# Kernel tuning notes

Hardware: AMD Instinct MI355X
Metric: run time of the kernel (lower is better)

The kernel has to match this reference:

```python
import jax, jax.numpy as jnp
import numpy as np

N = 50000
E = 800000
D_IN = 128
D_H = 128
N_CLASSES = 40
N_HIDDEN = 2


def _gcn_norm(edge_index, num_nodes):
    # Add self loops, compute symmetric normalization D^-1/2 (A+I) D^-1/2
    loops = jnp.arange(num_nodes, dtype=edge_index.dtype)
    src = jnp.concatenate([edge_index[0], loops])
    dst = jnp.concatenate([edge_index[1], loops])
    deg = jax.ops.segment_sum(jnp.ones_like(src, dtype=jnp.float32), dst,
                              num_segments=num_nodes)
    dinv = jnp.where(deg > 0, jax.lax.rsqrt(jnp.maximum(deg, 1.0)), 0.0)
    norm = dinv[src] * dinv[dst]  # [E+N]
    return src, dst, norm


def _gcn_conv(x, src, dst, norm, W, b):
    h = x @ W                          # [N, d_out] transform first (PyG order)
    msg = h[src] * norm[:, None]       # gather + scale, [E+N, d_out]
    out = jax.ops.segment_sum(msg, dst, num_segments=x.shape[0])
    return out + b


def setup_inputs() -> dict:
    key = jax.random.key(0)
    ks = jax.random.split(key, 8)
    x = jax.random.normal(ks[0], (N, D_IN), dtype=jnp.float32)
    edge_index = jax.random.randint(ks[1], (2, E), 0, N, dtype=jnp.int64)
    s = 1.0 / np.sqrt(D_IN)
    W1 = jax.random.uniform(ks[2], (D_IN, D_H), minval=-s, maxval=s, dtype=jnp.float32)
    b1 = jnp.zeros((D_H,), dtype=jnp.float32)
    sh = 1.0 / np.sqrt(D_H)
    Wh = jax.random.uniform(ks[3], (N_HIDDEN, D_H, D_H), minval=-sh, maxval=sh, dtype=jnp.float32)
    bh = jnp.zeros((N_HIDDEN, D_H), dtype=jnp.float32)
    Wf = jax.random.uniform(ks[4], (D_H, N_CLASSES), minval=-sh, maxval=sh, dtype=jnp.float32)
    bf = jnp.zeros((N_CLASSES,), dtype=jnp.float32)
    return {"x": x, "edge_index": edge_index, "W1": W1, "b1": b1,
            "Wh": Wh, "bh": bh, "Wf": Wf, "bf": bf}


def reference(x, edge_index, W1, b1, Wh, bh, Wf, bf):
    src, dst, norm = _gcn_norm(edge_index, x.shape[0])
    h = jax.nn.relu(_gcn_conv(x, src, dst, norm, W1, b1))
    for i in range(Wh.shape[0]):  # small fixed layer count
        h = jax.nn.relu(_gcn_conv(h, src, dst, norm, Wh[i], bh[i]))
    # extra relu in original forward is a no-op after relu above
    return h @ Wf + bf
```

## Files before the change

### kernel.cpp

```cpp
#include <hip/hip_runtime.h>

#define D 128
#define NC 40

typedef __attribute__((ext_vector_type(8))) short short8v;
typedef __attribute__((ext_vector_type(4))) float f32x4;

__device__ __forceinline__ unsigned short f2bf(float f) {
    unsigned u = __float_as_uint(f);
    u += 0x7fff + ((u >> 16) & 1);
    return (unsigned short)(u >> 16);
}
__device__ __forceinline__ float bf2f(unsigned short h) {
    return __uint_as_float(((unsigned)h) << 16);
}


__global__ void detect_kernel(const int* __restrict__ ei, int* __restrict__ flag) {
    __shared__ int any;
    if (threadIdx.x == 0) any = 0;
    __syncthreads();
    if (ei[threadIdx.x * 2 + 1] != 0) any = 1;
    __syncthreads();
    if (threadIdx.x == 0) *flag = (any == 0) ? 1 : 0;
}

__device__ __forceinline__ int load_idx(const int* ei, long long pos, int is64) {
    return is64 ? ei[pos * 2] : ei[pos];
}

__global__ void count_deg_kernel(const int* __restrict__ ei, const int* __restrict__ flag,
                                 int* __restrict__ deg, int E) {
    int e = blockIdx.x * blockDim.x + threadIdx.x;
    if (e >= E) return;
    int is64 = *flag;
    int d = load_idx(ei, (long long)E + e, is64);
    atomicAdd(&deg[d], 1);
}

__global__ void scan1_kernel(const int* __restrict__ deg, int* __restrict__ bsum, int n) {
    int i = blockIdx.x * 256 + threadIdx.x;
    int v = (i < n) ? deg[i] : 0;
    #pragma unroll
    for (int off = 32; off; off >>= 1) v += __shfl_down(v, off, 64);
    __shared__ int ws[4];
    if ((threadIdx.x & 63) == 0) ws[threadIdx.x >> 6] = v;
    __syncthreads();
    if (threadIdx.x == 0) bsum[blockIdx.x] = ws[0] + ws[1] + ws[2] + ws[3];
}

__global__ void scan2_kernel(int* __restrict__ bsum, int* __restrict__ total, int nb) {
    int t = threadIdx.x;
    int lane = t & 63, w = t >> 6;
    int v = (t < nb) ? bsum[t] : 0;
    int s = v;
    #pragma unroll
    for (int off = 1; off < 64; off <<= 1) {
        int x = __shfl_up(s, off, 64);
        if (lane >= off) s += x;
    }
    __shared__ int wsum[16];
    if (lane == 63) wsum[w] = s;
    __syncthreads();
    int wbase = 0;
    #pragma unroll
    for (int j = 0; j < 16; ++j) if (j < w) wbase += wsum[j];
    int excl = wbase + s - v;
    if (t < nb) bsum[t] = excl;
    if (t == nb - 1) *total = excl + v;
}

__global__ void scan3_kernel(const int* __restrict__ deg, const int* __restrict__ bsum,
                             const int* __restrict__ total, int* __restrict__ rowptr,
                             int* __restrict__ fill, float* __restrict__ dinv, int n) {
    int i = blockIdx.x * 256 + threadIdx.x;
    int v = (i < n) ? deg[i] : 0;
    int lane = threadIdx.x & 63, w = threadIdx.x >> 6;
    int s = v;
    #pragma unroll
    for (int off = 1; off < 64; off <<= 1) {
        int x = __shfl_up(s, off, 64);
        if (lane >= off) s += x;
    }
    __shared__ int wsum[4];
    if (lane == 63) wsum[w] = s;
    __syncthreads();
    int wbase = 0;
    #pragma unroll
    for (int j = 0; j < 4; ++j) if (j < w) wbase += wsum[j];
    int excl = bsum[blockIdx.x] + wbase + s - v;
    if (i < n) {
        rowptr[i] = excl;
        fill[i]   = excl;
        dinv[i]   = rsqrtf((float)(v + 1));
    }
    if (i == 0) rowptr[n] = *total;
}

__global__ void scatter_kernel(const int* __restrict__ ei, const int* __restrict__ flag,
                               int* __restrict__ fill, const float* __restrict__ dinv,
                               int2* __restrict__ col2, int E) {
    int e = blockIdx.x * blockDim.x + threadIdx.x;
    if (e >= E) return;
    int is64 = *flag;
    int s = load_idx(ei, (long long)e, is64);
    int d = load_idx(ei, (long long)E + e, is64);
    int pos = atomicAdd(&fill[d], 1);
    col2[pos] = make_int2(s, __float_as_int(dinv[s]));
}

__global__ void convertW_kernel(const float* __restrict__ W, unsigned short* __restrict__ hi,
                                unsigned short* __restrict__ lo, int N, int Npad) {
    int idx = blockIdx.x * blockDim.x + threadIdx.x;
    if (idx >= Npad * 128) return;
    int nn = idx >> 7, k = idx & 127;
    float v = (nn < N) ? W[k * N + nn] : 0.f;
    unsigned short h = f2bf(v);
    hi[idx] = h;
    lo[idx] = f2bf(v - bf2f(h));
}

__launch_bounds__(256)
__global__ void gemm128_mfma_kernel(const float* __restrict__ A, const unsigned short* __restrict__ Wcvt,
                                    float* __restrict__ C, int M) {
    __shared__ unsigned short Ah[64 * 128];
    __shared__ unsigned short Al[64 * 128];
    int t = threadIdx.x;
    int l = t & 63, w = t >> 6;
    int lr = l & 15, lh = l >> 4;

    const unsigned short* Whi = Wcvt;
    const unsigned short* Wlo = Wcvt + 128 * 128;
    short8v bhi[2][4], blo[2][4];
    int n0 = w * 32;
    #pragma unroll
    for (int ni = 0; ni < 2; ++ni) {
        int n = n0 + ni * 16 + lr;
        #pragma unroll
        for (int ks = 0; ks < 4; ++ks) {
            bhi[ni][ks] = *(const short8v*)&Whi[n * 128 + ks * 32 + lh * 8];
            blo[ni][ks] = *(const short8v*)&Wlo[n * 128 + ks * 32 + lh * 8];
        }
    }

    int row0 = blockIdx.x * 64;
    #pragma unroll
    for (int c = 0; c < 4; ++c) {
        int chunk = c * 256 + t;
        int r  = chunk >> 4;
        int kc = chunk & 15;
        int gr = row0 + r; if (gr >= M) gr = M - 1;
        float4 a0 = *(const float4*)&A[(size_t)gr * 128 + kc * 8];
        float4 a1 = *(const float4*)&A[(size_t)gr * 128 + kc * 8 + 4];
        float av[8] = {a0.x, a0.y, a0.z, a0.w, a1.x, a1.y, a1.z, a1.w};
        short8v hv, lv;
        #pragma unroll
        for (int j = 0; j < 8; ++j) {
            unsigned short hi = f2bf(av[j]);
            hv[j] = (short)hi;
            lv[j] = (short)f2bf(av[j] - bf2f(hi));
        }
        int off = (r << 8) + ((kc << 4) ^ ((r & 7) << 4));
        *(short8v*)((char*)Ah + off) = hv;
        *(short8v*)((char*)Al + off) = lv;
    }
    __syncthreads();

    f32x4 acc[4][2];
    #pragma unroll
    for (int mi = 0; mi < 4; ++mi)
        #pragma unroll
        for (int ni = 0; ni < 2; ++ni)
            acc[mi][ni] = (f32x4){0.f, 0.f, 0.f, 0.f};

    #pragma unroll
    for (int mi = 0; mi < 4; ++mi) {
        int row = mi * 16 + lr;
        #pragma unroll
        for (int ks = 0; ks < 4; ++ks) {
            int off = (row << 8) + (((ks << 6) + (lh << 4)) ^ ((row & 7) << 4));
            short8v ah = *(short8v*)((char*)Ah + off);
            short8v al = *(short8v*)((char*)Al + off);
            #pragma unroll
            for (int ni = 0; ni < 2; ++ni) {
                acc[mi][ni] = __builtin_amdgcn_mfma_f32_16x16x32_bf16(ah, bhi[ni][ks], acc[mi][ni], 0, 0, 0);
                acc[mi][ni] = __builtin_amdgcn_mfma_f32_16x16x32_bf16(ah, blo[ni][ks], acc[mi][ni], 0, 0, 0);
                acc[mi][ni] = __builtin_amdgcn_mfma_f32_16x16x32_bf16(al, bhi[ni][ks], acc[mi][ni], 0, 0, 0);
            }
        }
    }

    #pragma unroll
    for (int mi = 0; mi < 4; ++mi) {
        #pragma unroll
        for (int ni = 0; ni < 2; ++ni) {
            #pragma unroll
            for (int r = 0; r < 4; ++r) {
                int row = row0 + mi * 16 + lh * 4 + r;
                if (row < M) C[(size_t)row * 128 + n0 + ni * 16 + lr] = acc[mi][ni][r];
            }
        }
    }
}

__launch_bounds__(256)
__global__ void aggregate_kernel(const float4* __restrict__ h4, const float* __restrict__ dinv,
                                 const int* __restrict__ rowptr, const int2* __restrict__ col2,
                                 const float* __restrict__ bias, float4* __restrict__ out4, int n) {
    int node = blockIdx.x * 8 + (threadIdx.x >> 5);
    if (node >= n) return;
    int l = threadIdx.x & 31;
    float dn = dinv[node];
    size_t rowbase = (size_t)node * 32;
    float4 hv = h4[rowbase + l];
    float4 acc;
    acc.x = hv.x * dn; acc.y = hv.y * dn; acc.z = hv.z * dn; acc.w = hv.w * dn;
    int e = rowptr[node], e1 = rowptr[node + 1];
    int2 c[8];
    #pragma unroll
    for (int j = 0; j < 8; ++j)
        c[j] = (e + j < e1) ? col2[e + j] : make_int2(node, 0);
    while (e < e1) {
        int en = e + 8;
        int2 cn[8];
        #pragma unroll
        for (int j = 0; j < 8; ++j)
            cn[j] = (en + j < e1) ? col2[en + j] : make_int2(node, 0);
        float4 v[8];
        #pragma unroll
        for (int j = 0; j < 8; ++j) v[j] = h4[(size_t)c[j].x * 32 + l];
        #pragma unroll
        for (int j = 0; j < 8; ++j) {
            float ds = __int_as_float(c[j].y);
            acc.x += v[j].x * ds; acc.y += v[j].y * ds;
            acc.z += v[j].z * ds; acc.w += v[j].w * ds;
        }
        #pragma unroll
        for (int j = 0; j < 8; ++j) c[j] = cn[j];
        e = en;
    }
    float4 bv = *(const float4*)&bias[l * 4];
    float4 o;
    o.x = fmaxf(acc.x * dn + bv.x, 0.f);
    o.y = fmaxf(acc.y * dn + bv.y, 0.f);
    o.z = fmaxf(acc.z * dn + bv.z, 0.f);
    o.w = fmaxf(acc.w * dn + bv.w, 0.f);
    out4[rowbase + l] = o;
}

__launch_bounds__(256)
__global__ void final_mfma_kernel(const float* __restrict__ A, const unsigned short* __restrict__ Wcvt,
                                  const float* __restrict__ bf, float* __restrict__ C, int M) {
    __shared__ unsigned short Ah[64 * 128];
    __shared__ unsigned short Al[64 * 128];
    int t = threadIdx.x;
    int l = t & 63, w = t >> 6;
    int lr = l & 15, lh = l >> 4;

    const unsigned short* Whi = Wcvt;
    const unsigned short* Wlo = Wcvt + 48 * 128;
    short8v bhi[3][4], blo[3][4];
    #pragma unroll
    for (int nt = 0; nt < 3; ++nt) {
        int n = nt * 16 + lr;
        #pragma unroll
        for (int ks = 0; ks < 4; ++ks) {
            bhi[nt][ks] = *(const short8v*)&Whi[n * 128 + ks * 32 + lh * 8];
            blo[nt][ks] = *(const short8v*)&Wlo[n * 128 + ks * 32 + lh * 8];
        }
    }

    int row0 = blockIdx.x * 64;
    #pragma unroll
    for (int c = 0; c < 4; ++c) {
        int chunk = c * 256 + t;
        int r  = chunk >> 4;
        int kc = chunk & 15;
        int gr = row0 + r; if (gr >= M) gr = M - 1;
        float4 a0 = *(const float4*)&A[(size_t)gr * 128 + kc * 8];
        float4 a1 = *(const float4*)&A[(size_t)gr * 128 + kc * 8 + 4];
        float av[8] = {a0.x, a0.y, a0.z, a0.w, a1.x, a1.y, a1.z, a1.w};
        short8v hv, lv;
        #pragma unroll
        for (int j = 0; j < 8; ++j) {
            unsigned short hi = f2bf(av[j]);
            hv[j] = (short)hi;
            lv[j] = (short)f2bf(av[j] - bf2f(hi));
        }
        int off = (r << 8) + ((kc << 4) ^ ((r & 7) << 4));
        *(short8v*)((char*)Ah + off) = hv;
        *(short8v*)((char*)Al + off) = lv;
    }
    __syncthreads();

    f32x4 acc[3];
    #pragma unroll
    for (int nt = 0; nt < 3; ++nt) acc[nt] = (f32x4){0.f, 0.f, 0.f, 0.f};
    int row = w * 16 + lr;
    #pragma unroll
    for (int ks = 0; ks < 4; ++ks) {
        int off = (row << 8) + (((ks << 6) + (lh << 4)) ^ ((row & 7) << 4));
        short8v ah = *(short8v*)((char*)Ah + off);
        short8v al = *(short8v*)((char*)Al + off);
        #pragma unroll
        for (int nt = 0; nt < 3; ++nt) {
            acc[nt] = __builtin_amdgcn_mfma_f32_16x16x32_bf16(ah, bhi[nt][ks], acc[nt], 0, 0, 0);
            acc[nt] = __builtin_amdgcn_mfma_f32_16x16x32_bf16(ah, blo[nt][ks], acc[nt], 0, 0, 0);
            acc[nt] = __builtin_amdgcn_mfma_f32_16x16x32_bf16(al, bhi[nt][ks], acc[nt], 0, 0, 0);
        }
    }
    #pragma unroll
    for (int nt = 0; nt < 3; ++nt) {
        int col = nt * 16 + lr;
        #pragma unroll
        for (int r = 0; r < 4; ++r) {
            int ro = row0 + w * 16 + lh * 4 + r;
            if (col < NC && ro < M) C[(size_t)ro * NC + col] = acc[nt][r] + bf[col];
        }
    }
}

extern "C" void kernel_launch(void* const* d_in, const int* in_sizes, int n_in,
                              void* d_out, int out_size, void* d_ws, size_t ws_size,
                              hipStream_t stream) {
    const float* x  = (const float*)d_in[0];
    const int*   ei = (const int*)d_in[1];
    const float* W1 = (const float*)d_in[2];
    const float* b1 = (const float*)d_in[3];
    const float* Wh = (const float*)d_in[4];
    const float* bh = (const float*)d_in[5];
    const float* Wf = (const float*)d_in[6];
    const float* bf = (const float*)d_in[7];
    float* out = (float*)d_out;

    int n = in_sizes[0] / D;
    int E = in_sizes[1] / 2;

    char* ws = (char*)d_ws;
    size_t off = 0;
    auto alloc = [&](size_t bytes) {
        void* p = ws + off;
        off = (off + bytes + 255) & ~(size_t)255;
        return p;
    };
    float* B0     = (float*)alloc((size_t)n * D * 4);
    float* B1     = (float*)alloc((size_t)n * D * 4);
    int*   deg    = (int*)alloc((size_t)n * 4);
    int*   rowptr = (int*)alloc((size_t)(n + 1) * 4);
    int*   fill   = (int*)alloc((size_t)n * 4);
    int2*  col2   = (int2*)alloc((size_t)E * 8);
    float* dinv   = (float*)alloc((size_t)n * 4);
    int*   flag   = (int*)alloc(256);
    int*   bsum   = (int*)alloc(1024 * 4);
    int*   total  = (int*)alloc(256);
    unsigned short* Wc1  = (unsigned short*)alloc(2 * 128 * 128 * 2);
    unsigned short* Wch0 = (unsigned short*)alloc(2 * 128 * 128 * 2);
    unsigned short* Wch1 = (unsigned short*)alloc(2 * 128 * 128 * 2);
    unsigned short* Wcf  = (unsigned short*)alloc(2 * 48 * 128 * 2);

    int nb = (n + 255) / 256;

    hipMemsetAsync(deg, 0, (size_t)n * 4, stream);
    detect_kernel<<<1, 256, 0, stream>>>(ei, flag);
    count_deg_kernel<<<(E + 255) / 256, 256, 0, stream>>>(ei, flag, deg, E);
    scan1_kernel<<<nb, 256, 0, stream>>>(deg, bsum, n);
    scan2_kernel<<<1, 1024, 0, stream>>>(bsum, total, nb);
    scan3_kernel<<<nb, 256, 0, stream>>>(deg, bsum, total, rowptr, fill, dinv, n);
    scatter_kernel<<<(E + 255) / 256, 256, 0, stream>>>(ei, flag, fill, dinv, col2, E);

    convertW_kernel<<<(128 * 128 + 255) / 256, 256, 0, stream>>>(W1, Wc1, Wc1 + 128 * 128, 128, 128);
    convertW_kernel<<<(128 * 128 + 255) / 256, 256, 0, stream>>>(Wh, Wch0, Wch0 + 128 * 128, 128, 128);
    convertW_kernel<<<(128 * 128 + 255) / 256, 256, 0, stream>>>(Wh + 128 * 128, Wch1, Wch1 + 128 * 128, 128, 128);
    convertW_kernel<<<(48 * 128 + 255) / 256, 256, 0, stream>>>(Wf, Wcf, Wcf + 48 * 128, 40, 48);

    int gblocks = (n + 63) / 64;
    int agrid = (n + 7) / 8;

    gemm128_mfma_kernel<<<gblocks, 256, 0, stream>>>(x, Wc1, B0, n);
    aggregate_kernel<<<agrid, 256, 0, stream>>>((const float4*)B0, dinv, rowptr, col2, b1, (float4*)B1, n);
    gemm128_mfma_kernel<<<gblocks, 256, 0, stream>>>(B1, Wch0, B0, n);
    aggregate_kernel<<<agrid, 256, 0, stream>>>((const float4*)B0, dinv, rowptr, col2, bh, (float4*)B1, n);
    gemm128_mfma_kernel<<<gblocks, 256, 0, stream>>>(B1, Wch1, B0, n);
    aggregate_kernel<<<agrid, 256, 0, stream>>>((const float4*)B0, dinv, rowptr, col2, bh + D, (float4*)B1, n);
    final_mfma_kernel<<<gblocks, 256, 0, stream>>>(B1, Wcf, bf, out, n);
}
```

Baseline: 355.3 us.

## Bucket CSR neighbors by source-index chunk to improve gather locality

Builds the CSR with per-destination sub-buckets keyed by source node chunk (8192 nodes), so each node's neighbor list is roughly sorted by source range. This is meant to improve L2 locality of the feature gathers across concurrently running aggregate waves. Degree and dinv now come from the bucketed rowptr. The aggregate loop also drops its prefetch-with-padding scheme for 8/4/1 remainder loops, which avoids wasted padded gathers but loses the software prefetch of col indices. The setup scan grows to n*NCH entries.

```diff
diff --git a/kernel.cpp b/kernel.cpp
--- a/kernel.cpp
+++ b/kernel.cpp
@@ -2,6 +2,7 @@
 
 #define D 128
 #define NC 40
+#define CH_SHIFT 13
 
 typedef __attribute__((ext_vector_type(8))) short short8v;
 typedef __attribute__((ext_vector_type(4))) float f32x4;
@@ -29,24 +30,30 @@
     return is64 ? ei[pos * 2] : ei[pos];
 }
 
-__global__ void count_deg_kernel(const int* __restrict__ ei, const int* __restrict__ flag,
-                                 int* __restrict__ deg, int E) {
+__global__ void count_deg2_kernel(const int* __restrict__ ei, const int* __restrict__ flag,
+                                  int* __restrict__ deg2, int E, int NCH) {
     int e = blockIdx.x * blockDim.x + threadIdx.x;
     if (e >= E) return;
     int is64 = *flag;
+    int s = load_idx(ei, (long long)e, is64);
     int d = load_idx(ei, (long long)E + e, is64);
-    atomicAdd(&deg[d], 1);
-}
-
-__global__ void scan1_kernel(const int* __restrict__ deg, int* __restrict__ bsum, int n) {
-    int i = blockIdx.x * 256 + threadIdx.x;
-    int v = (i < n) ? deg[i] : 0;
+    atomicAdd(&deg2[(size_t)d * NCH + (s >> CH_SHIFT)], 1);
+}
+
+__global__ void scan1_kernel(const int* __restrict__ deg2, int* __restrict__ bsum, int m) {
+    int i = blockIdx.x * 512 + threadIdx.x;
+    int v = (i < m) ? deg2[i] : 0;
     #pragma unroll
     for (int off = 32; off; off >>= 1) v += __shfl_down(v, off, 64);
-    __shared__ int ws[4];
+    __shared__ int ws[8];
     if ((threadIdx.x & 63) == 0) ws[threadIdx.x >> 6] = v;
     __syncthreads();
-    if (threadIdx.x == 0) bsum[blockIdx.x] = ws[0] + ws[1] + ws[2] + ws[3];
+    if (threadIdx.x == 0) {
+        int s = 0;
+        #pragma unroll
+        for (int j = 0; j < 8; ++j) s += ws[j];
+        bsum[blockIdx.x] = s;
+    }
 }
 
 __global__ void scan2_kernel(int* __restrict__ bsum, int* __restrict__ total, int nb) {
@@ -70,11 +77,11 @@
     if (t == nb - 1) *total = excl + v;
 }
 
-__global__ void scan3_kernel(const int* __restrict__ deg, const int* __restrict__ bsum,
-                             const int* __restrict__ total, int* __restrict__ rowptr,
-                             int* __restrict__ fill, float* __restrict__ dinv, int n) {
-    int i = blockIdx.x * 256 + threadIdx.x;
-    int v = (i < n) ? deg[i] : 0;
+__global__ void scan3_kernel(const int* __restrict__ deg2, const int* __restrict__ bsum,
+                             const int* __restrict__ total, int* __restrict__ rowptr2,
+                             int* __restrict__ fill2, int m) {
+    int i = blockIdx.x * 512 + threadIdx.x;
+    int v = (i < m) ? deg2[i] : 0;
     int lane = threadIdx.x & 63, w = threadIdx.x >> 6;
     int s = v;
     #pragma unroll
@@ -82,30 +89,37 @@
         int x = __shfl_up(s, off, 64);
         if (lane >= off) s += x;
     }
-    __shared__ int wsum[4];
+    __shared__ int wsum[8];
     if (lane == 63) wsum[w] = s;
     __syncthreads();
     int wbase = 0;
     #pragma unroll
-    for (int j = 0; j < 4; ++j) if (j < w) wbase += wsum[j];
+    for (int j = 0; j < 8; ++j) if (j < w) wbase += wsum[j];
     int excl = bsum[blockIdx.x] + wbase + s - v;
-    if (i < n) {
-        rowptr[i] = excl;
-        fill[i]   = excl;
-        dinv[i]   = rsqrtf((float)(v + 1));
-    }
-    if (i == 0) rowptr[n] = *total;
+    if (i < m) {
+        rowptr2[i] = excl;
+        fill2[i]   = excl;
+    }
+    if (i == 0) rowptr2[m] = *total;
+}
+
+__global__ void dinv_kernel(const int* __restrict__ rowptr2, float* __restrict__ dinv,
+                            int n, int NCH) {
+    int i = blockIdx.x * 256 + threadIdx.x;
+    if (i >= n) return;
+    int deg = rowptr2[(size_t)(i + 1) * NCH] - rowptr2[(size_t)i * NCH];
+    dinv[i] = rsqrtf((float)(deg + 1));
 }
 
 __global__ void scatter_kernel(const int* __restrict__ ei, const int* __restrict__ flag,
-                               int* __restrict__ fill, const float* __restrict__ dinv,
-                               int2* __restrict__ col2, int E) {
+                               int* __restrict__ fill2, const float* __restrict__ dinv,
+                               int2* __restrict__ col2, int E, int NCH) {
     int e = blockIdx.x * blockDim.x + threadIdx.x;
     if (e >= E) return;
     int is64 = *flag;
     int s = load_idx(ei, (long long)e, is64);
     int d = load_idx(ei, (long long)E + e, is64);
-    int pos = atomicAdd(&fill[d], 1);
+    int pos = atomicAdd(&fill2[(size_t)d * NCH + (s >> CH_SHIFT)], 1);
     col2[pos] = make_int2(s, __float_as_int(dinv[s]));
 }
 
@@ -205,8 +219,9 @@
 
 __launch_bounds__(256)
 __global__ void aggregate_kernel(const float4* __restrict__ h4, const float* __restrict__ dinv,
-                                 const int* __restrict__ rowptr, const int2* __restrict__ col2,
-                                 const float* __restrict__ bias, float4* __restrict__ out4, int n) {
+                                 const int* __restrict__ rowptr2, const int2* __restrict__ col2,
+                                 const float* __restrict__ bias, float4* __restrict__ out4,
+                                 int n, int NCH) {
     int node = blockIdx.x * 8 + (threadIdx.x >> 5);
     if (node >= n) return;
     int l = threadIdx.x & 31;
@@ -215,17 +230,11 @@
     float4 hv = h4[rowbase + l];
     float4 acc;
     acc.x = hv.x * dn; acc.y = hv.y * dn; acc.z = hv.z * dn; acc.w = hv.w * dn;
-    int e = rowptr[node], e1 = rowptr[node + 1];
-    int2 c[8];
-    #pragma unroll
-    for (int j = 0; j < 8; ++j)
-        c[j] = (e + j < e1) ? col2[e + j] : make_int2(node, 0);
-    while (e < e1) {
-        int en = e + 8;
-        int2 cn[8];
-        #pragma unroll
-        for (int j = 0; j < 8; ++j)
-            cn[j] = (en + j < e1) ? col2[en + j] : make_int2(node, 0);
+    int e = rowptr2[(size_t)node * NCH], e1 = rowptr2[(size_t)(node + 1) * NCH];
+    for (; e + 8 <= e1; e += 8) {
+        int2 c[8];
+        #pragma unroll
+        for (int j = 0; j < 8; ++j) c[j] = col2[e + j];
         float4 v[8];
         #pragma unroll
         for (int j = 0; j < 8; ++j) v[j] = h4[(size_t)c[j].x * 32 + l];
@@ -235,9 +244,26 @@
             acc.x += v[j].x * ds; acc.y += v[j].y * ds;
             acc.z += v[j].z * ds; acc.w += v[j].w * ds;
         }
-        #pragma unroll
-        for (int j = 0; j < 8; ++j) c[j] = cn[j];
-        e = en;
+    }
+    for (; e + 4 <= e1; e += 4) {
+        int2 c[4];
+        #pragma unroll
+        for (int j = 0; j < 4; ++j) c[j] = col2[e + j];
+        float4 v[4];
+        #pragma unroll
+        for (int j = 0; j < 4; ++j) v[j] = h4[(size_t)c[j].x * 32 + l];
+        #pragma unroll
+        for (int j = 0; j < 4; ++j) {
+            float ds = __int_as_float(c[j].y);
+            acc.x += v[j].x * ds; acc.y += v[j].y * ds;
+            acc.z += v[j].z * ds; acc.w += v[j].w * ds;
+        }
+    }
+    for (; e < e1; ++e) {
+        int2 c = col2[e];
+        float ds = __int_as_float(c.y);
+        float4 v = h4[(size_t)c.x * 32 + l];
+        acc.x += v.x * ds; acc.y += v.y * ds; acc.z += v.z * ds; acc.w += v.w * ds;
     }
     float4 bv = *(const float4*)&bias[l * 4];
     float4 o;
@@ -335,6 +361,8 @@
 
     int n = in_sizes[0] / D;
     int E = in_sizes[1] / 2;
+    int NCH = (n + (1 << CH_SHIFT) - 1) >> CH_SHIFT;
+    int m = n * NCH;
 
     char* ws = (char*)d_ws;
     size_t off = 0;
@@ -345,9 +373,9 @@
     };
     float* B0     = (float*)alloc((size_t)n * D * 4);
     float* B1     = (float*)alloc((size_t)n * D * 4);
-    int*   deg    = (int*)alloc((size_t)n * 4);
-    int*   rowptr = (int*)alloc((size_t)(n + 1) * 4);
-    int*   fill   = (int*)alloc((size_t)n * 4);
+    int*   deg2   = (int*)alloc((size_t)m * 4);
+    int*   rowptr2= (int*)alloc((size_t)(m + 1) * 4);
+    int*   fill2  = (int*)alloc((size_t)m * 4);
     int2*  col2   = (int2*)alloc((size_t)E * 8);
     float* dinv   = (float*)alloc((size_t)n * 4);
     int*   flag   = (int*)alloc(256);
@@ -358,15 +386,16 @@
     unsigned short* Wch1 = (unsigned short*)alloc(2 * 128 * 128 * 2);
     unsigned short* Wcf  = (unsigned short*)alloc(2 * 48 * 128 * 2);
 
-    int nb = (n + 255) / 256;
-
-    hipMemsetAsync(deg, 0, (size_t)n * 4, stream);
+    int nb = (m + 511) / 512;
+
+    hipMemsetAsync(deg2, 0, (size_t)m * 4, stream);
     detect_kernel<<<1, 256, 0, stream>>>(ei, flag);
-    count_deg_kernel<<<(E + 255) / 256, 256, 0, stream>>>(ei, flag, deg, E);
-    scan1_kernel<<<nb, 256, 0, stream>>>(deg, bsum, n);
+    count_deg2_kernel<<<(E + 255) / 256, 256, 0, stream>>>(ei, flag, deg2, E, NCH);
+    scan1_kernel<<<nb, 512, 0, stream>>>(deg2, bsum, m);
     scan2_kernel<<<1, 1024, 0, stream>>>(bsum, total, nb);
-    scan3_kernel<<<nb, 256, 0, stream>>>(deg, bsum, total, rowptr, fill, dinv, n);
-    scatter_kernel<<<(E + 255) / 256, 256, 0, stream>>>(ei, flag, fill, dinv, col2, E);
+    scan3_kernel<<<nb, 512, 0, stream>>>(deg2, bsum, total, rowptr2, fill2, m);
+    dinv_kernel<<<(n + 255) / 256, 256, 0, stream>>>(rowptr2, dinv, n, NCH);
+    scatter_kernel<<<(E + 255) / 256, 256, 0, stream>>>(ei, flag, fill2, dinv, col2, E, NCH);
 
     convertW_kernel<<<(128 * 128 + 255) / 256, 256, 0, stream>>>(W1, Wc1, Wc1 + 128 * 128, 128, 128);
     convertW_kernel<<<(128 * 128 + 255) / 256, 256, 0, stream>>>(Wh, Wch0, Wch0 + 128 * 128, 128, 128);
@@ -377,10 +406,10 @@
     int agrid = (n + 7) / 8;
 
     gemm128_mfma_kernel<<<gblocks, 256, 0, stream>>>(x, Wc1, B0, n);
-    aggregate_kernel<<<agrid, 256, 0, stream>>>((const float4*)B0, dinv, rowptr, col2, b1, (float4*)B1, n);
+    aggregate_kernel<<<agrid, 256, 0, stream>>>((const float4*)B0, dinv, rowptr2, col2, b1, (float4*)B1, n, NCH);
     gemm128_mfma_kernel<<<gblocks, 256, 0, stream>>>(B1, Wch0, B0, n);
-    aggregate_kernel<<<agrid, 256, 0, stream>>>((const float4*)B0, dinv, rowptr, col2, bh, (float4*)B1, n);
+    aggregate_kernel<<<agrid, 256, 0, stream>>>((const float4*)B0, dinv, rowptr2, col2, bh, (float4*)B1, n, NCH);
     gemm128_mfma_kernel<<<gblocks, 256, 0, stream>>>(B1, Wch1, B0, n);
-    aggregate_kernel<<<agrid, 256, 0, stream>>>((const float4*)B0, dinv, rowptr, col2, bh + D, (float4*)B1, n);
+    aggregate_kernel<<<agrid, 256, 0, stream>>>((const float4*)B0, dinv, rowptr2, col2, bh + D, (float4*)B1, n, NCH);
     final_mfma_kernel<<<gblocks, 256, 0, stream>>>(B1, Wcf, bf, out, n);
 }
```

After: 347.0 us. 2.3% less time.

## Store intermediate activations as split bf16 hi/lo planes between GEMM and aggregation

Applied to the files above, without the earlier changes.

Intermediate node features are now kept as two bf16 planes (hi and lo residual) instead of fp32. GEMMs write the planes directly, aggregation reads and writes planes, and the downstream GEMMs load them into LDS without converting. This moves the fp32-to-split conversion out of each GEMM's load phase. It also merges the four weight-conversion launches into one and widens the scan blocks to 512 threads. The tradeoff is that aggregation now issues two gathers per neighbor (same total bytes) and does extra conversion arithmetic, and the aggregate prefetch pipeline was replaced by simpler chunked loops.

```diff
diff --git a/kernel.cpp b/kernel.cpp
--- a/kernel.cpp
+++ b/kernel.cpp
@@ -38,15 +38,20 @@
     atomicAdd(&deg[d], 1);
 }
 
-__global__ void scan1_kernel(const int* __restrict__ deg, int* __restrict__ bsum, int n) {
-    int i = blockIdx.x * 256 + threadIdx.x;
-    int v = (i < n) ? deg[i] : 0;
+__global__ void scan1_kernel(const int* __restrict__ deg, int* __restrict__ bsum, int m) {
+    int i = blockIdx.x * 512 + threadIdx.x;
+    int v = (i < m) ? deg[i] : 0;
     #pragma unroll
     for (int off = 32; off; off >>= 1) v += __shfl_down(v, off, 64);
-    __shared__ int ws[4];
+    __shared__ int ws[8];
     if ((threadIdx.x & 63) == 0) ws[threadIdx.x >> 6] = v;
     __syncthreads();
-    if (threadIdx.x == 0) bsum[blockIdx.x] = ws[0] + ws[1] + ws[2] + ws[3];
+    if (threadIdx.x == 0) {
+        int s = 0;
+        #pragma unroll
+        for (int j = 0; j < 8; ++j) s += ws[j];
+        bsum[blockIdx.x] = s;
+    }
 }
 
 __global__ void scan2_kernel(int* __restrict__ bsum, int* __restrict__ total, int nb) {
@@ -72,9 +77,9 @@
 
 __global__ void scan3_kernel(const int* __restrict__ deg, const int* __restrict__ bsum,
                              const int* __restrict__ total, int* __restrict__ rowptr,
-                             int* __restrict__ fill, float* __restrict__ dinv, int n) {
-    int i = blockIdx.x * 256 + threadIdx.x;
-    int v = (i < n) ? deg[i] : 0;
+                             int* __restrict__ fill, float* __restrict__ dinv, int m) {
+    int i = blockIdx.x * 512 + threadIdx.x;
+    int v = (i < m) ? deg[i] : 0;
     int lane = threadIdx.x & 63, w = threadIdx.x >> 6;
     int s = v;
     #pragma unroll
@@ -82,19 +87,19 @@
         int x = __shfl_up(s, off, 64);
         if (lane >= off) s += x;
     }
-    __shared__ int wsum[4];
+    __shared__ int wsum[8];
     if (lane == 63) wsum[w] = s;
     __syncthreads();
     int wbase = 0;
     #pragma unroll
-    for (int j = 0; j < 4; ++j) if (j < w) wbase += wsum[j];
+    for (int j = 0; j < 8; ++j) if (j < w) wbase += wsum[j];
     int excl = bsum[blockIdx.x] + wbase + s - v;
-    if (i < n) {
+    if (i < m) {
         rowptr[i] = excl;
         fill[i]   = excl;
         dinv[i]   = rsqrtf((float)(v + 1));
     }
-    if (i == 0) rowptr[n] = *total;
+    if (i == 0) rowptr[m] = *total;
 }
 
 __global__ void scatter_kernel(const int* __restrict__ ei, const int* __restrict__ flag,
@@ -109,20 +114,35 @@
     col2[pos] = make_int2(s, __float_as_int(dinv[s]));
 }
 
-__global__ void convertW_kernel(const float* __restrict__ W, unsigned short* __restrict__ hi,
-                                unsigned short* __restrict__ lo, int N, int Npad) {
-    int idx = blockIdx.x * blockDim.x + threadIdx.x;
-    if (idx >= Npad * 128) return;
-    int nn = idx >> 7, k = idx & 127;
-    float v = (nn < N) ? W[k * N + nn] : 0.f;
-    unsigned short h = f2bf(v);
-    hi[idx] = h;
-    lo[idx] = f2bf(v - bf2f(h));
-}
+__global__ void convertW_all_kernel(const float* __restrict__ W1, const float* __restrict__ Wh,
+                                    const float* __restrict__ Wf,
+                                    unsigned short* __restrict__ Wc1, unsigned short* __restrict__ Wch0,
+                                    unsigned short* __restrict__ Wch1, unsigned short* __restrict__ Wcf) {
+    int idx = blockIdx.x * 256 + threadIdx.x;
+    if (idx < 49152) {
+        int which = idx >> 14;
+        int j = idx & 16383;
+        int nn = j >> 7, k = j & 127;
+        const float* W = (which == 0) ? W1 : (which == 1) ? Wh : Wh + 16384;
+        unsigned short* o = (which == 0) ? Wc1 : (which == 1) ? Wch0 : Wch1;
+        float v = W[k * 128 + nn];
+        unsigned short h = f2bf(v);
+        o[j] = h;
+        o[16384 + j] = f2bf(v - bf2f(h));
+    } else if (idx < 49152 + 6144) {
+        int j = idx - 49152;
+        int nn = j >> 7, k = j & 127;
+        float v = (nn < NC) ? Wf[k * NC + nn] : 0.f;
+        unsigned short h = f2bf(v);
+        Wcf[j] = h;
+        Wcf[6144 + j] = f2bf(v - bf2f(h));
+    }
+}
+
 
 __launch_bounds__(256)
-__global__ void gemm128_mfma_kernel(const float* __restrict__ A, const unsigned short* __restrict__ Wcvt,
-                                    float* __restrict__ C, int M) {
+__global__ void gemm128_f32in_kernel(const float* __restrict__ A, const unsigned short* __restrict__ Wcvt,
+                                     unsigned short* __restrict__ Chi, unsigned short* __restrict__ Clo, int M) {
     __shared__ unsigned short Ah[64 * 128];
     __shared__ unsigned short Al[64 * 128];
     int t = threadIdx.x;
@@ -197,60 +217,186 @@
             #pragma unroll
             for (int r = 0; r < 4; ++r) {
                 int row = row0 + mi * 16 + lh * 4 + r;
-                if (row < M) C[(size_t)row * 128 + n0 + ni * 16 + lr] = acc[mi][ni][r];
+                if (row < M) {
+                    float v = acc[mi][ni][r];
+                    unsigned short h = f2bf(v);
+                    size_t o = (size_t)row * 128 + n0 + ni * 16 + lr;
+                    Chi[o] = h;
+                    Clo[o] = f2bf(v - bf2f(h));
+                }
             }
         }
     }
 }
 
 __launch_bounds__(256)
-__global__ void aggregate_kernel(const float4* __restrict__ h4, const float* __restrict__ dinv,
+__global__ void gemm128_planes_kernel(const unsigned short* __restrict__ Ahi_g,
+                                      const unsigned short* __restrict__ Alo_g,
+                                      const unsigned short* __restrict__ Wcvt,
+                                      unsigned short* __restrict__ Chi, unsigned short* __restrict__ Clo, int M) {
+    __shared__ unsigned short Ah[64 * 128];
+    __shared__ unsigned short Al[64 * 128];
+    int t = threadIdx.x;
+    int l = t & 63, w = t >> 6;
+    int lr = l & 15, lh = l >> 4;
+
+    const unsigned short* Whi = Wcvt;
+    const unsigned short* Wlo = Wcvt + 128 * 128;
+    short8v bhi[2][4], blo[2][4];
+    int n0 = w * 32;
+    #pragma unroll
+    for (int ni = 0; ni < 2; ++ni) {
+        int n = n0 + ni * 16 + lr;
+        #pragma unroll
+        for (int ks = 0; ks < 4; ++ks) {
+            bhi[ni][ks] = *(const short8v*)&Whi[n * 128 + ks * 32 + lh * 8];
+            blo[ni][ks] = *(const short8v*)&Wlo[n * 128 + ks * 32 + lh * 8];
+        }
+    }
+
+    int row0 = blockIdx.x * 64;
+    #pragma unroll
+    for (int c = 0; c < 4; ++c) {
+        int chunk = c * 256 + t;
+        int r  = chunk >> 4;
+        int kc = chunk & 15;
+        int gr = row0 + r; if (gr >= M) gr = M - 1;
+        int off = (r << 8) + ((kc << 4) ^ ((r & 7) << 4));
+        *(short8v*)((char*)Ah + off) = *(const short8v*)&Ahi_g[(size_t)gr * 128 + kc * 8];
+        *(short8v*)((char*)Al + off) = *(const short8v*)&Alo_g[(size_t)gr * 128 + kc * 8];
+    }
+    __syncthreads();
+
+    f32x4 acc[4][2];
+    #pragma unroll
+    for (int mi = 0; mi < 4; ++mi)
+        #pragma unroll
+        for (int ni = 0; ni < 2; ++ni)
+            acc[mi][ni] = (f32x4){0.f, 0.f, 0.f, 0.f};
+
+    #pragma unroll
+    for (int mi = 0; mi < 4; ++mi) {
+        int row = mi * 16 + lr;
+        #pragma unroll
+        for (int ks = 0; ks < 4; ++ks) {
+            int off = (row << 8) + (((ks << 6) + (lh << 4)) ^ ((row & 7) << 4));
+            short8v ah = *(short8v*)((char*)Ah + off);
+            short8v al = *(short8v*)((char*)Al + off);
+            #pragma unroll
+            for (int ni = 0; ni < 2; ++ni) {
+                acc[mi][ni] = __builtin_amdgcn_mfma_f32_16x16x32_bf16(ah, bhi[ni][ks], acc[mi][ni], 0, 0, 0);
+                acc[mi][ni] = __builtin_amdgcn_mfma_f32_16x16x32_bf16(ah, blo[ni][ks], acc[mi][ni], 0, 0, 0);
+                acc[mi][ni] = __builtin_amdgcn_mfma_f32_16x16x32_bf16(al, bhi[ni][ks], acc[mi][ni], 0, 0, 0);
+            }
+        }
+    }
+
+    #pragma unroll
+    for (int mi = 0; mi < 4; ++mi) {
+        #pragma unroll
+        for (int ni = 0; ni < 2; ++ni) {
+            #pragma unroll
+            for (int r = 0; r < 4; ++r) {
+                int row = row0 + mi * 16 + lh * 4 + r;
+                if (row < M) {
+                    float v = acc[mi][ni][r];
+                    unsigned short h = f2bf(v);
+                    size_t o = (size_t)row * 128 + n0 + ni * 16 + lr;
+                    Chi[o] = h;
+                    Clo[o] = f2bf(v - bf2f(h));
+                }
+            }
+        }
+    }
+}
+
+__launch_bounds__(256)
+__global__ void aggregate_kernel(const ushort4* __restrict__ hhi, const ushort4* __restrict__ hlo,
+                                 const float* __restrict__ dinv,
                                  const int* __restrict__ rowptr, const int2* __restrict__ col2,
-                                 const float* __restrict__ bias, float4* __restrict__ out4, int n) {
+                                 const float* __restrict__ bias,
+                                 ushort4* __restrict__ ohi, ushort4* __restrict__ olo, int n) {
     int node = blockIdx.x * 8 + (threadIdx.x >> 5);
     if (node >= n) return;
     int l = threadIdx.x & 31;
     float dn = dinv[node];
     size_t rowbase = (size_t)node * 32;
-    float4 hv = h4[rowbase + l];
+    ushort4 sh = hhi[rowbase + l], sl = hlo[rowbase + l];
     float4 acc;
-    acc.x = hv.x * dn; acc.y = hv.y * dn; acc.z = hv.z * dn; acc.w = hv.w * dn;
+    acc.x = (bf2f(sh.x) + bf2f(sl.x)) * dn;
+    acc.y = (bf2f(sh.y) + bf2f(sl.y)) * dn;
+    acc.z = (bf2f(sh.z) + bf2f(sl.z)) * dn;
+    acc.w = (bf2f(sh.w) + bf2f(sl.w)) * dn;
     int e = rowptr[node], e1 = rowptr[node + 1];
-    int2 c[8];
-    #pragma unroll
-    for (int j = 0; j < 8; ++j)
-        c[j] = (e + j < e1) ? col2[e + j] : make_int2(node, 0);
-    while (e < e1) {
-        int en = e + 8;
-        int2 cn[8];
-        #pragma unroll
-        for (int j = 0; j < 8; ++j)
-            cn[j] = (en + j < e1) ? col2[en + j] : make_int2(node, 0);
-        float4 v[8];
-        #pragma unroll
-        for (int j = 0; j < 8; ++j) v[j] = h4[(size_t)c[j].x * 32 + l];
+    for (; e + 8 <= e1; e += 8) {
+        int2 c[8];
+        #pragma unroll
+        for (int j = 0; j < 8; ++j) c[j] = col2[e + j];
+        ushort4 vh[8], vl[8];
+        #pragma unroll
+        for (int j = 0; j < 8; ++j) {
+            size_t b = (size_t)c[j].x * 32 + l;
+            vh[j] = hhi[b];
+            vl[j] = hlo[b];
+        }
         #pragma unroll
         for (int j = 0; j < 8; ++j) {
             float ds = __int_as_float(c[j].y);
-            acc.x += v[j].x * ds; acc.y += v[j].y * ds;
-            acc.z += v[j].z * ds; acc.w += v[j].w * ds;
-        }
-        #pragma unroll
-        for (int j = 0; j < 8; ++j) c[j] = cn[j];
-        e = en;
+            acc.x += bf2f(vh[j].x) * ds; acc.y += bf2f(vh[j].y) * ds;
+            acc.z += bf2f(vh[j].z) * ds; acc.w += bf2f(vh[j].w) * ds;
+            acc.x += bf2f(vl[j].x) * ds; acc.y += bf2f(vl[j].y) * ds;
+            acc.z += bf2f(vl[j].z) * ds; acc.w += bf2f(vl[j].w) * ds;
+        }
+    }
+    for (; e + 4 <= e1; e += 4) {
+        int2 c[4];
+        #pragma unroll
+        for (int j = 0; j < 4; ++j) c[j] = col2[e + j];
+        ushort4 vh[4], vl[4];
+        #pragma unroll
+        for (int j = 0; j < 4; ++j) {
+            size_t b = (size_t)c[j].x * 32 + l;
+            vh[j] = hhi[b];
+            vl[j] = hlo[b];
+        }
+        #pragma unroll
+        for (int j = 0; j < 4; ++j) {
+            float ds = __int_as_float(c[j].y);
+            acc.x += bf2f(vh[j].x) * ds; acc.y += bf2f(vh[j].y) * ds;
+            acc.z += bf2f(vh[j].z) * ds; acc.w += bf2f(vh[j].w) * ds;
+            acc.x += bf2f(vl[j].x) * ds; acc.y += bf2f(vl[j].y) * ds;
+            acc.z += bf2f(vl[j].z) * ds; acc.w += bf2f(vl[j].w) * ds;
+        }
+    }
+    for (; e < e1; ++e) {
+        int2 c = col2[e];
+        float ds = __int_as_float(c.y);
+        size_t b = (size_t)c.x * 32 + l;
+        ushort4 vh = hhi[b], vl = hlo[b];
+        acc.x += (bf2f(vh.x) + bf2f(vl.x)) * ds;
+        acc.y += (bf2f(vh.y) + bf2f(vl.y)) * ds;
+        acc.z += (bf2f(vh.z) + bf2f(vl.z)) * ds;
+        acc.w += (bf2f(vh.w) + bf2f(vl.w)) * ds;
     }
     float4 bv = *(const float4*)&bias[l * 4];
-    float4 o;
-    o.x = fmaxf(acc.x * dn + bv.x, 0.f);
-    o.y = fmaxf(acc.y * dn + bv.y, 0.f);
-    o.z = fmaxf(acc.z * dn + bv.z, 0.f);
-    o.w = fmaxf(acc.w * dn + bv.w, 0.f);
-    out4[rowbase + l] = o;
+    float ox = fmaxf(acc.x * dn + bv.x, 0.f);
+    float oy = fmaxf(acc.y * dn + bv.y, 0.f);
+    float oz = fmaxf(acc.z * dn + bv.z, 0.f);
+    float ow = fmaxf(acc.w * dn + bv.w, 0.f);
+    ushort4 oh, ol;
+    oh.x = f2bf(ox); ol.x = f2bf(ox - bf2f(oh.x));
+    oh.y = f2bf(oy); ol.y = f2bf(oy - bf2f(oh.y));
+    oh.z = f2bf(oz); ol.z = f2bf(oz - bf2f(oh.z));
+    oh.w = f2bf(ow); ol.w = f2bf(ow - bf2f(oh.w));
+    ohi[rowbase + l] = oh;
+    olo[rowbase + l] = ol;
 }
 
 __launch_bounds__(256)
-__global__ void final_mfma_kernel(const float* __restrict__ A, const unsigned short* __restrict__ Wcvt,
-                                  const float* __restrict__ bf, float* __restrict__ C, int M) {
+__global__ void final_planes_kernel(const unsigned short* __restrict__ Ahi_g,
+                                    const unsigned short* __restrict__ Alo_g,
+                                    const unsigned short* __restrict__ Wcvt,
+                                    const float* __restrict__ bf, float* __restrict__ C, int M) {
     __shared__ unsigned short Ah[64 * 128];
     __shared__ unsigned short Al[64 * 128];
     int t = threadIdx.x;
@@ -277,19 +423,9 @@
         int r  = chunk >> 4;
         int kc = chunk & 15;
         int gr = row0 + r; if (gr >= M) gr = M - 1;
-        float4 a0 = *(const float4*)&A[(size_t)gr * 128 + kc * 8];
-        float4 a1 = *(const float4*)&A[(size_t)gr * 128 + kc * 8 + 4];
-        float av[8] = {a0.x, a0.y, a0.z, a0.w, a1.x, a1.y, a1.z, a1.w};
-        short8v hv, lv;
-        #pragma unroll
-        for (int j = 0; j < 8; ++j) {
-            unsigned short hi = f2bf(av[j]);
-            hv[j] = (short)hi;
-            lv[j] = (short)f2bf(av[j] - bf2f(hi));
-        }
         int off = (r << 8) + ((kc << 4) ^ ((r & 7) << 4));
-        *(short8v*)((char*)Ah + off) = hv;
-        *(short8v*)((char*)Al + off) = lv;
+        *(short8v*)((char*)Ah + off) = *(const short8v*)&Ahi_g[(size_t)gr * 128 + kc * 8];
+        *(short8v*)((char*)Al + off) = *(const short8v*)&Alo_g[(size_t)gr * 128 + kc * 8];
     }
     __syncthreads();
 
@@ -343,8 +479,10 @@
         off = (off + bytes + 255) & ~(size_t)255;
         return p;
     };
-    float* B0     = (float*)alloc((size_t)n * D * 4);
-    float* B1     = (float*)alloc((size_t)n * D * 4);
+    unsigned short* P0hi = (unsigned short*)alloc((size_t)n * D * 2);
+    unsigned short* P0lo = (unsigned short*)alloc((size_t)n * D * 2);
+    unsigned short* P1hi = (unsigned short*)alloc((size_t)n * D * 2);
+    unsigned short* P1lo = (unsigned short*)alloc((size_t)n * D * 2);
     int*   deg    = (int*)alloc((size_t)n * 4);
     int*   rowptr = (int*)alloc((size_t)(n + 1) * 4);
     int*   fill   = (int*)alloc((size_t)n * 4);
@@ -358,29 +496,28 @@
     unsigned short* Wch1 = (unsigned short*)alloc(2 * 128 * 128 * 2);
     unsigned short* Wcf  = (unsigned short*)alloc(2 * 48 * 128 * 2);
 
-    int nb = (n + 255) / 256;
+    int nb = (n + 511) / 512;
 
     hipMemsetAsync(deg, 0, (size_t)n * 4, stream);
     detect_kernel<<<1, 256, 0, stream>>>(ei, flag);
     count_deg_kernel<<<(E + 255) / 256, 256, 0, stream>>>(ei, flag, deg, E);
-    scan1_kernel<<<nb, 256, 0, stream>>>(deg, bsum, n);
+    scan1_kernel<<<nb, 512, 0, stream>>>(deg, bsum, n);
     scan2_kernel<<<1, 1024, 0, stream>>>(bsum, total, nb);
-    scan3_kernel<<<nb, 256, 0, stream>>>(deg, bsum, total, rowptr, fill, dinv, n);
+    scan3_kernel<<<nb, 512, 0, stream>>>(deg, bsum, total, rowptr, fill, dinv, n);
     scatter_kernel<<<(E + 255) / 256, 256, 0, stream>>>(ei, flag, fill, dinv, col2, E);
-
-    convertW_kernel<<<(128 * 128 + 255) / 256, 256, 0, stream>>>(W1, Wc1, Wc1 + 128 * 128, 128, 128);
-    convertW_kernel<<<(128 * 128 + 255) / 256, 256, 0, stream>>>(Wh, Wch0, Wch0 + 128 * 128, 128, 128);
-    convertW_kernel<<<(128 * 128 + 255) / 256, 256, 0, stream>>>(Wh + 128 * 128, Wch1, Wch1 + 128 * 128, 128, 128);
-    convertW_kernel<<<(48 * 128 + 255) / 256, 256, 0, stream>>>(Wf, Wcf, Wcf + 48 * 128, 40, 48);
+    convertW_all_kernel<<<(49152 + 6144 + 255) / 256, 256, 0, stream>>>(W1, Wh, Wf, Wc1, Wch0, Wch1, Wcf);
 
     int gblocks = (n + 63) / 64;
     int agrid = (n + 7) / 8;
 
-    gemm128_mfma_kernel<<<gblocks, 256, 0, stream>>>(x, Wc1, B0, n);
-    aggregate_kernel<<<agrid, 256, 0, stream>>>((const float4*)B0, dinv, rowptr, col2, b1, (float4*)B1, n);
-    gemm128_mfma_kernel<<<gblocks, 256, 0, stream>>>(B1, Wch0, B0, n);
-    aggregate_kernel<<<agrid, 256, 0, stream>>>((const float4*)B0, dinv, rowptr, col2, bh, (float4*)B1, n);
-    gemm128_mfma_kernel<<<gblocks, 256, 0, stream>>>(B1, Wch1, B0, n);
-    aggregate_kernel<<<agrid, 256, 0, stream>>>((const float4*)B0, dinv, rowptr, col2, bh + D, (float4*)B1, n);
-    final_mfma_kernel<<<gblocks, 256, 0, stream>>>(B1, Wcf, bf, out, n);
-}
+    gemm128_f32in_kernel<<<gblocks, 256, 0, stream>>>(x, Wc1, P0hi, P0lo, n);
+    aggregate_kernel<<<agrid, 256, 0, stream>>>((const ushort4*)P0hi, (const ushort4*)P0lo, dinv, rowptr, col2, b1,
+                                                (ushort4*)P1hi, (ushort4*)P1lo, n);
+    gemm128_planes_kernel<<<gblocks, 256, 0, stream>>>(P1hi, P1lo, Wch0, P0hi, P0lo, n);
+    aggregate_kernel<<<agrid, 256, 0, stream>>>((const ushort4*)P0hi, (const ushort4*)P0lo, dinv, rowptr, col2, bh,
+                                                (ushort4*)P1hi, (ushort4*)P1lo, n);
+    gemm128_planes_kernel<<<gblocks, 256, 0, stream>>>(P1hi, P1lo, Wch1, P0hi, P0lo, n);
+    aggregate_kernel<<<agrid, 256, 0, stream>>>((const ushort4*)P0hi, (const ushort4*)P0lo, dinv, rowptr, col2, bh + D,
+                                                (ushort4*)P1hi, (ushort4*)P1lo, n);
+    final_planes_kernel<<<gblocks, 256, 0, stream>>>(P1hi, P1lo, Wcf, bf, out, n);
+}
```

After: 354.2 us. About the same (-0.3%).
